# Kernel tuning notes

Measured on AMD Instinct MI355X. Metric: run time of the kernel, lower is better.

## Reference

```python
import jax, jax.numpy as jnp
import numpy as np
from jax import lax

T, B, D, H = 1024, 64, 512, 1024


def setup_inputs() -> dict:
    key = jax.random.key(0)
    ks = jax.random.split(key, 5)
    x = jax.random.normal(ks[0], (T, B, D), dtype=jnp.float32)
    W_ih_0 = jax.random.normal(ks[1], (H, D), dtype=jnp.float32) * (1.0 / np.sqrt(D))
    w_hh_0 = jax.random.uniform(ks[2], (H,), dtype=jnp.float32)
    b_0 = jnp.zeros((H,), dtype=jnp.float32)
    W_ih_1 = jax.random.normal(ks[3], (H, H), dtype=jnp.float32) * (1.0 / np.sqrt(H))
    w_hh_1 = jax.random.uniform(ks[4], (H,), dtype=jnp.float32)
    b_1 = jnp.zeros((H,), dtype=jnp.float32)
    return {"x": x, "W_ih_0": W_ih_0, "w_hh_0": w_hh_0, "b_0": b_0,
            "W_ih_1": W_ih_1, "w_hh_1": w_hh_1, "b_1": b_1}


def _indrnn_layer(x, W_ih, w_hh, b):
    # Hoist the input projection into one batched GEMM over all timesteps.
    pre = jnp.einsum('tbd,hd->tbh', x, W_ih) + b  # [T,B,H]
    h0 = jnp.zeros((x.shape[1], W_ih.shape[0]), dtype=x.dtype)

    def step(h, p):
        h_new = jnp.tanh(p + h * w_hh)  # diagonal recurrence
        return h_new, h_new

    _, out = lax.scan(step, h0, pre)  # out: [T,B,H]
    return out


def reference(x, W_ih_0, w_hh_0, b_0, W_ih_1, w_hh_1, b_1):
    out0 = _indrnn_layer(x, W_ih_0, w_hh_0, b_0)
    out1 = _indrnn_layer(out0, W_ih_1, w_hh_1, b_1)
    # Original returns (last-layer outputs, initial hidden) -- hidden is
    # the unchanged zeros tensor of shape [num_layers, B, H].
    hidden = jnp.zeros((2, x.shape[1], W_ih_0.shape[0]), dtype=x.dtype)
    return out1, hidden
```

## Files before the change

### kernel.cpp

```cpp
#include <hip/hip_runtime.h>
#include <hip/hip_fp16.h>
#include <cstdint>
#include <cstddef>

#define TT 1024
#define BB 64
#define DD 512
#define HH 1024
#define MM (TT * BB)

typedef _Float16 f16;
typedef _Float16 f16x8 __attribute__((ext_vector_type(8)));
typedef float f32x4 __attribute__((ext_vector_type(4)));

__global__ void cvt_f32_to_f16(const float* __restrict__ src,
                               f16* __restrict__ dst, int n) {
    int i = blockIdx.x * blockDim.x + threadIdx.x;
    int idx = i * 8;
    if (idx + 8 <= n) {
        float4 a = *reinterpret_cast<const float4*>(src + idx);
        float4 b = *reinterpret_cast<const float4*>(src + idx + 4);
        f16x8 o;
        o[0] = (f16)a.x; o[1] = (f16)a.y; o[2] = (f16)a.z; o[3] = (f16)a.w;
        o[4] = (f16)b.x; o[5] = (f16)b.y; o[6] = (f16)b.z; o[7] = (f16)b.w;
        *reinterpret_cast<f16x8*>(dst + idx) = o;
    } else {
        for (int k = idx; k < n; ++k) dst[k] = (f16)src[k];
    }
}

__device__ __forceinline__ void gload16(const void* g, void* l) {
    __builtin_amdgcn_global_load_lds(
        (const __attribute__((address_space(1))) void*)g,
        (__attribute__((address_space(3))) void*)l, 16, 0, 0);
}

__device__ __forceinline__ void stage_tile(const f16* __restrict__ G,
                                           int rowbase, int K, int ktile,
                                           f16* lbuf, int tid) {
    #pragma unroll
    for (int j = 0; j < 2; ++j) {
        int p = (j * 512 + tid) * 16;
        int L = p ^ (((p >> 6) & 3) << 4);
        int row  = L >> 6;
        int colB = L & 63;
        const f16* g = G + (size_t)(rowbase + row) * K + ktile * 32 + (colB >> 1);
        gload16(g, (char*)lbuf + p);
    }
}

template <typename TC>
__global__ __launch_bounds__(512, 2) void gemm2(
    const f16* __restrict__ A, const f16* __restrict__ W,
    const float* __restrict__ bias, TC* __restrict__ C,
    int M, int N, int K) {
    __shared__ f16 Abuf[4][256 * 32];
    __shared__ f16 Bbuf[4][256 * 32];

    const int tid  = threadIdx.x;
    const int lane = tid & 63;
    const int wid  = tid >> 6;
    const int wm   = wid >> 2;
    const int wn   = wid & 3;
    const int lr   = lane & 15;
    const int cswz = ((lane >> 4) << 4) ^ ((lr & 3) << 4);

    const int nwg = gridDim.x;
    int bid = blockIdx.x;
    int wg  = (nwg % 8 == 0) ? ((bid & 7) * (nwg >> 3) + (bid >> 3)) : bid;
    const int ncol = N >> 8;
    const int brow = (wg / ncol) << 8;
    const int bcol = (wg % ncol) << 8;

    const int NT = K >> 5;

    f32x4 acc[8][4] = {};

    for (int u = 0; u < 3; ++u) {
        stage_tile(A, brow, K, u, Abuf[u], tid);
        stage_tile(W, bcol, K, u, Bbuf[u], tid);
    }
    asm volatile("s_waitcnt vmcnt(8)" ::: "memory");
    __builtin_amdgcn_s_barrier();

    for (int t = 0; t < NT; ++t) {
        const f16* As = Abuf[t & 3];
        const f16* Bs = Bbuf[t & 3];
        f16x8 bf[4], af[4];
        #pragma unroll
        for (int fn = 0; fn < 4; ++fn) {
            int r = wn * 64 + fn * 16 + lr;
            bf[fn] = *reinterpret_cast<const f16x8*>((const char*)Bs + r * 64 + cswz);
        }
        #pragma unroll
        for (int i = 0; i < 4; ++i) {
            int r = wm * 128 + i * 16 + lr;
            af[i] = *reinterpret_cast<const f16x8*>((const char*)As + r * 64 + cswz);
        }
        if (t + 3 < NT) stage_tile(A, brow, K, t + 3, Abuf[(t + 3) & 3], tid);
        __builtin_amdgcn_s_barrier();
        __builtin_amdgcn_s_setprio(1);
        #pragma unroll
        for (int i = 0; i < 4; ++i)
            #pragma unroll
            for (int fn = 0; fn < 4; ++fn)
                acc[i][fn] = __builtin_amdgcn_mfma_f32_16x16x32_f16(
                    af[i], bf[fn], acc[i][fn], 0, 0, 0);
        __builtin_amdgcn_s_setprio(0);
        __builtin_amdgcn_s_barrier();

        #pragma unroll
        for (int i = 0; i < 4; ++i) {
            int r = wm * 128 + (4 + i) * 16 + lr;
            af[i] = *reinterpret_cast<const f16x8*>((const char*)As + r * 64 + cswz);
        }
        if (t + 3 < NT) stage_tile(W, bcol, K, t + 3, Bbuf[(t + 3) & 3], tid);
        __builtin_amdgcn_s_barrier();
        __builtin_amdgcn_s_setprio(1);
        #pragma unroll
        for (int i = 0; i < 4; ++i)
            #pragma unroll
            for (int fn = 0; fn < 4; ++fn)
                acc[4 + i][fn] = __builtin_amdgcn_mfma_f32_16x16x32_f16(
                    af[i], bf[fn], acc[4 + i][fn], 0, 0, 0);
        __builtin_amdgcn_s_setprio(0);
        if (t + 3 < NT)      { asm volatile("s_waitcnt vmcnt(8)" ::: "memory"); }
        else if (t + 2 < NT) { asm volatile("s_waitcnt vmcnt(4)" ::: "memory"); }
        else                 { asm volatile("s_waitcnt vmcnt(0)" ::: "memory"); }
        __builtin_amdgcn_s_barrier();
    }

    #pragma unroll
    for (int fn = 0; fn < 4; ++fn) {
        int col = bcol + wn * 64 + fn * 16 + lr;
        float bv = bias[col];
        #pragma unroll
        for (int fm = 0; fm < 8; ++fm) {
            int row0 = brow + wm * 128 + fm * 16 + (lane >> 4) * 4;
            #pragma unroll
            for (int j = 0; j < 4; ++j) {
                C[(size_t)(row0 + j) * N + col] = (TC)(acc[fm][fn][j] + bv);
            }
        }
    }
}

__device__ __forceinline__ float fast_tanh(float x) {
    float e = __builtin_amdgcn_exp2f(x * 2.8853900817779268f);
    float r = __builtin_amdgcn_rcpf(e + 1.0f);
    return 1.0f - 2.0f * r;
}

template <typename TI, typename TO, int PF>
__global__ __launch_bounds__(256) void scan_kernel(
    const TI* __restrict__ pre, const float* __restrict__ w,
    TO* __restrict__ out) {
    const int S = BB * HH;
    const int idx = blockIdx.x * blockDim.x + threadIdx.x;
    const float wv = w[idx & (HH - 1)];
    const TI* p = pre + idx;
    TO* o = out + idx;

    float buf[PF];
    #pragma unroll
    for (int i = 0; i < PF; ++i) buf[i] = (float)p[(size_t)i * S];

    float h = 0.f;
    for (int t0 = 0; t0 < TT; t0 += PF) {
        float nbuf[PF];
        #pragma unroll
        for (int i = 0; i < PF; ++i) {
            int tp = t0 + PF + i;
            tp = (tp < TT - 1) ? tp : (TT - 1);
            nbuf[i] = (float)p[(size_t)tp * S];
        }
        #pragma unroll
        for (int i = 0; i < PF; ++i) {
            h = fast_tanh(fmaf(h, wv, buf[i]));
            o[(size_t)(t0 + i) * S] = (TO)h;
        }
        #pragma unroll
        for (int i = 0; i < PF; ++i) buf[i] = nbuf[i];
    }
}

__global__ void zero_kernel(float* p, int n) {
    int i = blockIdx.x * blockDim.x + threadIdx.x;
    if (i < n) p[i] = 0.f;
}

extern "C" void kernel_launch(void* const* d_in, const int* in_sizes, int n_in,
                              void* d_out, int out_size, void* d_ws, size_t ws_size,
                              hipStream_t stream) {
    const float* x  = (const float*)d_in[0];
    const float* W0 = (const float*)d_in[1];
    const float* w0 = (const float*)d_in[2];
    const float* b0 = (const float*)d_in[3];
    const float* W1 = (const float*)d_in[4];
    const float* w1 = (const float*)d_in[5];
    const float* b1 = (const float*)d_in[6];
    float* out = (float*)d_out;

    const size_t SZ_big = (size_t)MM * HH * sizeof(f16);
    const size_t O_W0   = SZ_big;
    const size_t O_W1   = O_W0 + (size_t)HH * DD * sizeof(f16);
    const size_t O_pre1 = O_W1 + (size_t)HH * HH * sizeof(f16);
    const bool f16pre1  = (ws_size >= O_pre1 + SZ_big);

    f16* big   = (f16*)d_ws;
    f16* W0h   = (f16*)((char*)d_ws + O_W0);
    f16* W1h   = (f16*)((char*)d_ws + O_W1);
    f16* pre1h = (f16*)((char*)d_ws + O_pre1);

    const int nwg = (MM / 256) * (HH / 256);

    cvt_f32_to_f16<<<(MM * DD) / 8 / 256, 256, 0, stream>>>(x, big, MM * DD);
    cvt_f32_to_f16<<<(HH * DD) / 8 / 256, 256, 0, stream>>>(W0, W0h, HH * DD);
    cvt_f32_to_f16<<<(HH * HH) / 8 / 256, 256, 0, stream>>>(W1, W1h, HH * HH);

    gemm2<f16><<<nwg, 512, 0, stream>>>(big, W0h, b0, (f16*)d_out, MM, HH, DD);

    scan_kernel<f16, f16, 32><<<(BB * HH) / 256, 256, 0, stream>>>(
        (const f16*)d_out, w0, big);

    if (f16pre1) {
        gemm2<f16><<<nwg, 512, 0, stream>>>(big, W1h, b1, pre1h, MM, HH, HH);
        scan_kernel<f16, float, 32><<<(BB * HH) / 256, 256, 0, stream>>>(
            pre1h, w1, out);
    } else {
        gemm2<float><<<nwg, 512, 0, stream>>>(big, W1h, b1, out, MM, HH, HH);
        scan_kernel<float, float, 32><<<(BB * HH) / 256, 256, 0, stream>>>(
            out, w1, out);
    }

    zero_kernel<<<(2 * BB * HH) / 256, 256, 0, stream>>>(
        out + (size_t)MM * HH, 2 * BB * HH);
}
```

Baseline: 499.6 us.

## Deepen GEMM K-tile to 64 with double buffering and LDS-staged f16 epilogue

```diff
diff --git a/kernel.cpp b/kernel.cpp
--- a/kernel.cpp
+++ b/kernel.cpp
@@ -35,27 +35,31 @@
         (__attribute__((address_space(3))) void*)l, 16, 0, 0);
 }
 
-__device__ __forceinline__ void stage_tile(const f16* __restrict__ G,
-                                           int rowbase, int K, int ktile,
-                                           f16* lbuf, int tid) {
+__device__ __forceinline__ void stage64(const f16* __restrict__ G,
+                                        int rowbase, int K, int kt,
+                                        f16* lbuf, int tid) {
     #pragma unroll
-    for (int j = 0; j < 2; ++j) {
-        int p = (j * 512 + tid) * 16;
-        int L = p ^ (((p >> 6) & 3) << 4);
-        int row  = L >> 6;
-        int colB = L & 63;
-        const f16* g = G + (size_t)(rowbase + row) * K + ktile * 32 + (colB >> 1);
-        gload16(g, (char*)lbuf + p);
-    }
+    for (int j = 0; j < 4; ++j) {
+        int p   = (j * 512 + tid) * 16;
+        int row = p >> 7;
+        int lc  = (p & 127) ^ ((row & 7) << 4);
+        gload16(G + (size_t)(rowbase + row) * K + kt * 64 + (lc >> 1),
+                (char*)lbuf + p);
+    }
+}
+
+__device__ __forceinline__ f16x8 ldfrag(const f16* buf, int r, int s,
+                                        int kg, int lr) {
+    int c = ((s * 4 + kg) ^ (lr & 7)) << 4;
+    return *reinterpret_cast<const f16x8*>((const char*)buf + r * 128 + c);
 }
 
 template <typename TC>
-__global__ __launch_bounds__(512, 2) void gemm2(
+__global__ __launch_bounds__(512, 2) void gemm3(
     const f16* __restrict__ A, const f16* __restrict__ W,
     const float* __restrict__ bias, TC* __restrict__ C,
     int M, int N, int K) {
-    __shared__ f16 Abuf[4][256 * 32];
-    __shared__ f16 Bbuf[4][256 * 32];
+    __shared__ f16 lds[2][2][256 * 64];
 
     const int tid  = threadIdx.x;
     const int lane = tid & 63;
@@ -63,7 +67,7 @@
     const int wm   = wid >> 2;
     const int wn   = wid & 3;
     const int lr   = lane & 15;
-    const int cswz = ((lane >> 4) << 4) ^ ((lr & 3) << 4);
+    const int kg   = lane >> 4;
 
     const int nwg = gridDim.x;
     int bid = blockIdx.x;
@@ -72,74 +76,143 @@
     const int brow = (wg / ncol) << 8;
     const int bcol = (wg % ncol) << 8;
 
-    const int NT = K >> 5;
+    const int NT = K >> 6;
 
     f32x4 acc[8][4] = {};
-
-    for (int u = 0; u < 3; ++u) {
-        stage_tile(A, brow, K, u, Abuf[u], tid);
-        stage_tile(W, bcol, K, u, Bbuf[u], tid);
-    }
+    f16x8 aA[4][2], b0[2][2], b1[2][2];
+
+    stage64(A, brow, K, 0, lds[0][0], tid);
+    stage64(W, bcol, K, 0, lds[1][0], tid);
+    stage64(A, brow, K, 1, lds[0][1], tid);
+    stage64(W, bcol, K, 1, lds[1][1], tid);
     asm volatile("s_waitcnt vmcnt(8)" ::: "memory");
     __builtin_amdgcn_s_barrier();
 
     for (int t = 0; t < NT; ++t) {
-        const f16* As = Abuf[t & 3];
-        const f16* Bs = Bbuf[t & 3];
-        f16x8 bf[4], af[4];
+        const f16* As = lds[0][t & 1];
+        const f16* Bs = lds[1][t & 1];
+        const bool st = (t + 2 < NT);
+
+        #pragma unroll
+        for (int i = 0; i < 4; ++i)
+            #pragma unroll
+            for (int s = 0; s < 2; ++s)
+                aA[i][s] = ldfrag(As, wm * 128 + i * 16 + lr, s, kg, lr);
+        #pragma unroll
+        for (int n = 0; n < 2; ++n)
+            #pragma unroll
+            for (int s = 0; s < 2; ++s)
+                b0[n][s] = ldfrag(Bs, wn * 64 + n * 16 + lr, s, kg, lr);
+        __builtin_amdgcn_s_barrier();
+        asm volatile("s_waitcnt lgkmcnt(0)" ::: "memory");
+        __builtin_amdgcn_s_setprio(1);
+        #pragma unroll
+        for (int i = 0; i < 4; ++i)
+            #pragma unroll
+            for (int n = 0; n < 2; ++n)
+                #pragma unroll
+                for (int s = 0; s < 2; ++s)
+                    acc[i][n] = __builtin_amdgcn_mfma_f32_16x16x32_f16(
+                        aA[i][s], b0[n][s], acc[i][n], 0, 0, 0);
+        __builtin_amdgcn_s_setprio(0);
+        __builtin_amdgcn_s_barrier();
+
+        #pragma unroll
+        for (int n = 0; n < 2; ++n)
+            #pragma unroll
+            for (int s = 0; s < 2; ++s)
+                b1[n][s] = ldfrag(Bs, wn * 64 + (2 + n) * 16 + lr, s, kg, lr);
+        __builtin_amdgcn_s_barrier();
+        asm volatile("s_waitcnt lgkmcnt(0)" ::: "memory");
+        __builtin_amdgcn_s_setprio(1);
+        #pragma unroll
+        for (int i = 0; i < 4; ++i)
+            #pragma unroll
+            for (int n = 0; n < 2; ++n)
+                #pragma unroll
+                for (int s = 0; s < 2; ++s)
+                    acc[i][2 + n] = __builtin_amdgcn_mfma_f32_16x16x32_f16(
+                        aA[i][s], b1[n][s], acc[i][2 + n], 0, 0, 0);
+        __builtin_amdgcn_s_setprio(0);
+        __builtin_amdgcn_s_barrier();
+
+        #pragma unroll
+        for (int i = 0; i < 4; ++i)
+            #pragma unroll
+            for (int s = 0; s < 2; ++s)
+                aA[i][s] = ldfrag(As, wm * 128 + (4 + i) * 16 + lr, s, kg, lr);
+        if (st) stage64(W, bcol, K, t + 2, lds[1][t & 1], tid);
+        __builtin_amdgcn_s_barrier();
+        asm volatile("s_waitcnt lgkmcnt(0)" ::: "memory");
+        __builtin_amdgcn_s_setprio(1);
+        #pragma unroll
+        for (int i = 0; i < 4; ++i)
+            #pragma unroll
+            for (int n = 0; n < 2; ++n)
+                #pragma unroll
+                for (int s = 0; s < 2; ++s)
+                    acc[4 + i][n] = __builtin_amdgcn_mfma_f32_16x16x32_f16(
+                        aA[i][s], b0[n][s], acc[4 + i][n], 0, 0, 0);
+        __builtin_amdgcn_s_setprio(0);
+        __builtin_amdgcn_s_barrier();
+
+        if (st) stage64(A, brow, K, t + 2, lds[0][t & 1], tid);
+        __builtin_amdgcn_s_barrier();
+        __builtin_amdgcn_s_setprio(1);
+        #pragma unroll
+        for (int i = 0; i < 4; ++i)
+            #pragma unroll
+            for (int n = 0; n < 2; ++n)
+                #pragma unroll
+                for (int s = 0; s < 2; ++s)
+                    acc[4 + i][2 + n] = __builtin_amdgcn_mfma_f32_16x16x32_f16(
+                        aA[i][s], b1[n][s], acc[4 + i][2 + n], 0, 0, 0);
+        __builtin_amdgcn_s_setprio(0);
+        if (st)                { asm volatile("s_waitcnt vmcnt(8)" ::: "memory"); }
+        else if (t + 1 < NT)   { asm volatile("s_waitcnt vmcnt(0)" ::: "memory"); }
+        __builtin_amdgcn_s_barrier();
+    }
+
+    if constexpr (sizeof(TC) == 2) {
+        f16* Ct = &lds[0][0][0];
         #pragma unroll
         for (int fn = 0; fn < 4; ++fn) {
-            int r = wn * 64 + fn * 16 + lr;
-            bf[fn] = *reinterpret_cast<const f16x8*>((const char*)Bs + r * 64 + cswz);
-        }
-        #pragma unroll
-        for (int i = 0; i < 4; ++i) {
-            int r = wm * 128 + i * 16 + lr;
-            af[i] = *reinterpret_cast<const f16x8*>((const char*)As + r * 64 + cswz);
-        }
-        if (t + 3 < NT) stage_tile(A, brow, K, t + 3, Abuf[(t + 3) & 3], tid);
-        __builtin_amdgcn_s_barrier();
-        __builtin_amdgcn_s_setprio(1);
-        #pragma unroll
-        for (int i = 0; i < 4; ++i)
-            #pragma unroll
-            for (int fn = 0; fn < 4; ++fn)
-                acc[i][fn] = __builtin_amdgcn_mfma_f32_16x16x32_f16(
-                    af[i], bf[fn], acc[i][fn], 0, 0, 0);
-        __builtin_amdgcn_s_setprio(0);
-        __builtin_amdgcn_s_barrier();
-
-        #pragma unroll
-        for (int i = 0; i < 4; ++i) {
-            int r = wm * 128 + (4 + i) * 16 + lr;
-            af[i] = *reinterpret_cast<const f16x8*>((const char*)As + r * 64 + cswz);
-        }
-        if (t + 3 < NT) stage_tile(W, bcol, K, t + 3, Bbuf[(t + 3) & 3], tid);
-        __builtin_amdgcn_s_barrier();
-        __builtin_amdgcn_s_setprio(1);
-        #pragma unroll
-        for (int i = 0; i < 4; ++i)
-            #pragma unroll
-            for (int fn = 0; fn < 4; ++fn)
-                acc[4 + i][fn] = __builtin_amdgcn_mfma_f32_16x16x32_f16(
-                    af[i], bf[fn], acc[4 + i][fn], 0, 0, 0);
-        __builtin_amdgcn_s_setprio(0);
-        if (t + 3 < NT)      { asm volatile("s_waitcnt vmcnt(8)" ::: "memory"); }
-        else if (t + 2 < NT) { asm volatile("s_waitcnt vmcnt(4)" ::: "memory"); }
-        else                 { asm volatile("s_waitcnt vmcnt(0)" ::: "memory"); }
-        __builtin_amdgcn_s_barrier();
-    }
-
-    #pragma unroll
-    for (int fn = 0; fn < 4; ++fn) {
-        int col = bcol + wn * 64 + fn * 16 + lr;
-        float bv = bias[col];
-        #pragma unroll
-        for (int fm = 0; fm < 8; ++fm) {
-            int row0 = brow + wm * 128 + fm * 16 + (lane >> 4) * 4;
-            #pragma unroll
-            for (int j = 0; j < 4; ++j) {
-                C[(size_t)(row0 + j) * N + col] = (TC)(acc[fm][fn][j] + bv);
+            int col = wn * 64 + fn * 16 + lr;
+            float bv = bias[bcol + col];
+            #pragma unroll
+            for (int fm = 0; fm < 8; ++fm) {
+                int row0 = wm * 128 + fm * 16 + kg * 4;
+                #pragma unroll
+                for (int j = 0; j < 4; ++j) {
+                    int r  = row0 + j;
+                    int pb = r * 512 + ((col * 2) ^ ((r & 7) << 4));
+                    *(f16*)((char*)Ct + pb) = (f16)(acc[fm][fn][j] + bv);
+                }
+            }
+        }
+        __builtin_amdgcn_s_barrier();
+        asm volatile("s_waitcnt lgkmcnt(0)" ::: "memory");
+        #pragma unroll
+        for (int i = 0; i < 16; ++i) {
+            int e   = (i * 512 + tid) * 16;
+            int row = e >> 9;
+            int cb  = e & 511;
+            int pb  = row * 512 + (cb ^ ((row & 7) << 4));
+            f16x8 v = *(const f16x8*)((const char*)Ct + pb);
+            *reinterpret_cast<f16x8*>(
+                (f16*)C + (size_t)(brow + row) * N + bcol + (cb >> 1)) = v;
+        }
+    } else {
+        #pragma unroll
+        for (int fn = 0; fn < 4; ++fn) {
+            int col = bcol + wn * 64 + fn * 16 + lr;
+            float bv = bias[col];
+            #pragma unroll
+            for (int fm = 0; fm < 8; ++fm) {
+                int row0 = brow + wm * 128 + fm * 16 + kg * 4;
+                #pragma unroll
+                for (int j = 0; j < 4; ++j)
+                    C[(size_t)(row0 + j) * N + col] = (TC)(acc[fm][fn][j] + bv);
             }
         }
     }
@@ -218,17 +291,17 @@
     cvt_f32_to_f16<<<(HH * DD) / 8 / 256, 256, 0, stream>>>(W0, W0h, HH * DD);
     cvt_f32_to_f16<<<(HH * HH) / 8 / 256, 256, 0, stream>>>(W1, W1h, HH * HH);
 
-    gemm2<f16><<<nwg, 512, 0, stream>>>(big, W0h, b0, (f16*)d_out, MM, HH, DD);
+    gemm3<f16><<<nwg, 512, 0, stream>>>(big, W0h, b0, (f16*)d_out, MM, HH, DD);
 
     scan_kernel<f16, f16, 32><<<(BB * HH) / 256, 256, 0, stream>>>(
         (const f16*)d_out, w0, big);
 
     if (f16pre1) {
-        gemm2<f16><<<nwg, 512, 0, stream>>>(big, W1h, b1, pre1h, MM, HH, HH);
+        gemm3<f16><<<nwg, 512, 0, stream>>>(big, W1h, b1, pre1h, MM, HH, HH);
         scan_kernel<f16, float, 32><<<(BB * HH) / 256, 256, 0, stream>>>(
             pre1h, w1, out);
     } else {
-        gemm2<float><<<nwg, 512, 0, stream>>>(big, W1h, b1, out, MM, HH, HH);
+        gemm3<float><<<nwg, 512, 0, stream>>>(big, W1h, b1, out, MM, HH, HH);
         scan_kernel<float, float, 32><<<(BB * HH) / 256, 256, 0, stream>>>(
             out, w1, out);
     }
```

Measured after the change: 435.4 us. 12.8% less time.

## Replace 256x256 pipelined GEMM with 128x128 single-buffer GEMM and LDS-staged epilogue

Applied to the files above, without the earlier changes.

```diff
diff --git a/kernel.cpp b/kernel.cpp
--- a/kernel.cpp
+++ b/kernel.cpp
@@ -35,111 +35,115 @@
         (__attribute__((address_space(3))) void*)l, 16, 0, 0);
 }
 
-__device__ __forceinline__ void stage_tile(const f16* __restrict__ G,
-                                           int rowbase, int K, int ktile,
-                                           f16* lbuf, int tid) {
+__device__ __forceinline__ void stage128x64(const f16* __restrict__ G,
+                                            int rowbase, int K, int kt,
+                                            f16* lbuf, int tid) {
     #pragma unroll
-    for (int j = 0; j < 2; ++j) {
-        int p = (j * 512 + tid) * 16;
-        int L = p ^ (((p >> 6) & 3) << 4);
-        int row  = L >> 6;
-        int colB = L & 63;
-        const f16* g = G + (size_t)(rowbase + row) * K + ktile * 32 + (colB >> 1);
-        gload16(g, (char*)lbuf + p);
-    }
+    for (int j = 0; j < 4; ++j) {
+        int p   = (j * 256 + tid) * 16;
+        int row = p >> 7;
+        int lc  = (p & 127) ^ ((row & 7) << 4);
+        gload16(G + (size_t)(rowbase + row) * K + kt * 64 + (lc >> 1),
+                (char*)lbuf + p);
+    }
+}
+
+__device__ __forceinline__ f16x8 ldfrag(const f16* buf, int r, int s,
+                                        int kg) {
+    int c = ((s * 4 + kg) ^ (r & 7)) << 4;
+    return *reinterpret_cast<const f16x8*>((const char*)buf + r * 128 + c);
 }
 
 template <typename TC>
-__global__ __launch_bounds__(512, 2) void gemm2(
+__global__ __launch_bounds__(256, 4) void gemm5(
     const f16* __restrict__ A, const f16* __restrict__ W,
     const float* __restrict__ bias, TC* __restrict__ C,
     int M, int N, int K) {
-    __shared__ f16 Abuf[4][256 * 32];
-    __shared__ f16 Bbuf[4][256 * 32];
+    __shared__ f16 lds[2][128 * 64];
 
     const int tid  = threadIdx.x;
     const int lane = tid & 63;
     const int wid  = tid >> 6;
-    const int wm   = wid >> 2;
-    const int wn   = wid & 3;
+    const int wm   = wid >> 1;
+    const int wn   = wid & 1;
     const int lr   = lane & 15;
-    const int cswz = ((lane >> 4) << 4) ^ ((lr & 3) << 4);
+    const int kg   = lane >> 4;
 
     const int nwg = gridDim.x;
     int bid = blockIdx.x;
     int wg  = (nwg % 8 == 0) ? ((bid & 7) * (nwg >> 3) + (bid >> 3)) : bid;
-    const int ncol = N >> 8;
-    const int brow = (wg / ncol) << 8;
-    const int bcol = (wg % ncol) << 8;
-
-    const int NT = K >> 5;
-
-    f32x4 acc[8][4] = {};
-
-    for (int u = 0; u < 3; ++u) {
-        stage_tile(A, brow, K, u, Abuf[u], tid);
-        stage_tile(W, bcol, K, u, Bbuf[u], tid);
-    }
-    asm volatile("s_waitcnt vmcnt(8)" ::: "memory");
-    __builtin_amdgcn_s_barrier();
+    const int ncol = N >> 7;
+    const int brow = (wg / ncol) << 7;
+    const int bcol = (wg % ncol) << 7;
+
+    const int NT = K >> 6;
+
+    f32x4 acc[4][4] = {};
 
     for (int t = 0; t < NT; ++t) {
-        const f16* As = Abuf[t & 3];
-        const f16* Bs = Bbuf[t & 3];
-        f16x8 bf[4], af[4];
+        __syncthreads();
+        stage128x64(A, brow, K, t, lds[0], tid);
+        stage128x64(W, bcol, K, t, lds[1], tid);
+        __syncthreads();
+
+        #pragma unroll
+        for (int s = 0; s < 2; ++s) {
+            f16x8 af[4], bf[4];
+            #pragma unroll
+            for (int m = 0; m < 4; ++m)
+                af[m] = ldfrag(lds[0], wm * 64 + m * 16 + lr, s, kg);
+            #pragma unroll
+            for (int n = 0; n < 4; ++n)
+                bf[n] = ldfrag(lds[1], wn * 64 + n * 16 + lr, s, kg);
+            #pragma unroll
+            for (int m = 0; m < 4; ++m)
+                #pragma unroll
+                for (int n = 0; n < 4; ++n)
+                    acc[m][n] = __builtin_amdgcn_mfma_f32_16x16x32_f16(
+                        af[m], bf[n], acc[m][n], 0, 0, 0);
+        }
+    }
+
+    if constexpr (sizeof(TC) == 2) {
+        f16* Ct = &lds[0][0];
+        __syncthreads();
         #pragma unroll
         for (int fn = 0; fn < 4; ++fn) {
-            int r = wn * 64 + fn * 16 + lr;
-            bf[fn] = *reinterpret_cast<const f16x8*>((const char*)Bs + r * 64 + cswz);
-        }
-        #pragma unroll
-        for (int i = 0; i < 4; ++i) {
-            int r = wm * 128 + i * 16 + lr;
-            af[i] = *reinterpret_cast<const f16x8*>((const char*)As + r * 64 + cswz);
-        }
-        if (t + 3 < NT) stage_tile(A, brow, K, t + 3, Abuf[(t + 3) & 3], tid);
-        __builtin_amdgcn_s_barrier();
-        __builtin_amdgcn_s_setprio(1);
-        #pragma unroll
-        for (int i = 0; i < 4; ++i)
-            #pragma unroll
-            for (int fn = 0; fn < 4; ++fn)
-                acc[i][fn] = __builtin_amdgcn_mfma_f32_16x16x32_f16(
-                    af[i], bf[fn], acc[i][fn], 0, 0, 0);
-        __builtin_amdgcn_s_setprio(0);
-        __builtin_amdgcn_s_barrier();
-
-        #pragma unroll
-        for (int i = 0; i < 4; ++i) {
-            int r = wm * 128 + (4 + i) * 16 + lr;
-            af[i] = *reinterpret_cast<const f16x8*>((const char*)As + r * 64 + cswz);
-        }
-        if (t + 3 < NT) stage_tile(W, bcol, K, t + 3, Bbuf[(t + 3) & 3], tid);
-        __builtin_amdgcn_s_barrier();
-        __builtin_amdgcn_s_setprio(1);
-        #pragma unroll
-        for (int i = 0; i < 4; ++i)
-            #pragma unroll
-            for (int fn = 0; fn < 4; ++fn)
-                acc[4 + i][fn] = __builtin_amdgcn_mfma_f32_16x16x32_f16(
-                    af[i], bf[fn], acc[4 + i][fn], 0, 0, 0);
-        __builtin_amdgcn_s_setprio(0);
-        if (t + 3 < NT)      { asm volatile("s_waitcnt vmcnt(8)" ::: "memory"); }
-        else if (t + 2 < NT) { asm volatile("s_waitcnt vmcnt(4)" ::: "memory"); }
-        else                 { asm volatile("s_waitcnt vmcnt(0)" ::: "memory"); }
-        __builtin_amdgcn_s_barrier();
-    }
-
-    #pragma unroll
-    for (int fn = 0; fn < 4; ++fn) {
-        int col = bcol + wn * 64 + fn * 16 + lr;
-        float bv = bias[col];
-        #pragma unroll
-        for (int fm = 0; fm < 8; ++fm) {
-            int row0 = brow + wm * 128 + fm * 16 + (lane >> 4) * 4;
-            #pragma unroll
-            for (int j = 0; j < 4; ++j) {
-                C[(size_t)(row0 + j) * N + col] = (TC)(acc[fm][fn][j] + bv);
+            int col = wn * 64 + fn * 16 + lr;
+            float bv = bias[bcol + col];
+            #pragma unroll
+            for (int fm = 0; fm < 4; ++fm) {
+                int row0 = wm * 64 + fm * 16 + kg * 4;
+                #pragma unroll
+                for (int j = 0; j < 4; ++j) {
+                    int r  = row0 + j;
+                    int pb = r * 256 + ((col * 2) ^ ((r & 7) << 4));
+                    *(f16*)((char*)Ct + pb) = (f16)(acc[fm][fn][j] + bv);
+                }
+            }
+        }
+        __syncthreads();
+        #pragma unroll
+        for (int i = 0; i < 8; ++i) {
+            int e   = (i * 256 + tid) * 16;
+            int row = e >> 8;
+            int cb  = e & 255;
+            int pb  = row * 256 + (cb ^ ((row & 7) << 4));
+            f16x8 v = *(const f16x8*)((const char*)Ct + pb);
+            *reinterpret_cast<f16x8*>(
+                (f16*)C + (size_t)(brow + row) * N + bcol + (cb >> 1)) = v;
+        }
+    } else {
+        #pragma unroll
+        for (int fn = 0; fn < 4; ++fn) {
+            int col = bcol + wn * 64 + fn * 16 + lr;
+            float bv = bias[col];
+            #pragma unroll
+            for (int fm = 0; fm < 4; ++fm) {
+                int row0 = brow + wm * 64 + fm * 16 + kg * 4;
+                #pragma unroll
+                for (int j = 0; j < 4; ++j)
+                    C[(size_t)(row0 + j) * N + col] = (TC)(acc[fm][fn][j] + bv);
             }
         }
     }
@@ -212,23 +216,23 @@
     f16* W1h   = (f16*)((char*)d_ws + O_W1);
     f16* pre1h = (f16*)((char*)d_ws + O_pre1);
 
-    const int nwg = (MM / 256) * (HH / 256);
+    const int nwg = (MM / 128) * (HH / 128);
 
     cvt_f32_to_f16<<<(MM * DD) / 8 / 256, 256, 0, stream>>>(x, big, MM * DD);
     cvt_f32_to_f16<<<(HH * DD) / 8 / 256, 256, 0, stream>>>(W0, W0h, HH * DD);
     cvt_f32_to_f16<<<(HH * HH) / 8 / 256, 256, 0, stream>>>(W1, W1h, HH * HH);
 
-    gemm2<f16><<<nwg, 512, 0, stream>>>(big, W0h, b0, (f16*)d_out, MM, HH, DD);
+    gemm5<f16><<<nwg, 256, 0, stream>>>(big, W0h, b0, (f16*)d_out, MM, HH, DD);
 
     scan_kernel<f16, f16, 32><<<(BB * HH) / 256, 256, 0, stream>>>(
         (const f16*)d_out, w0, big);
 
     if (f16pre1) {
-        gemm2<f16><<<nwg, 512, 0, stream>>>(big, W1h, b1, pre1h, MM, HH, HH);
+        gemm5<f16><<<nwg, 256, 0, stream>>>(big, W1h, b1, pre1h, MM, HH, HH);
         scan_kernel<f16, float, 32><<<(BB * HH) / 256, 256, 0, stream>>>(
             pre1h, w1, out);
     } else {
-        gemm2<float><<<nwg, 512, 0, stream>>>(big, W1h, b1, out, MM, HH, HH);
+        gemm5<float><<<nwg, 256, 0, stream>>>(big, W1h, b1, out, MM, HH, HH);
         scan_kernel<float, float, 32><<<(BB * HH) / 256, 256, 0, stream>>>(
             out, w1, out);
     }
```

Result: faster. 427.1 us (-14.5%).
